# Kernel tuning notes

Measured on AMD Instinct MI355X. Metric: run time of the kernel, lower is better.

The kernel has to match this reference:

```python
import jax, jax.numpy as jnp
import numpy as np

# Rows of A/B form separable 3x3 filters via outer product:
#   f0 = identity, f1 = sobel_y, f2 = sobel_x
_A = np.array([[0, 1, 0], [1, 0, -1], [1, 2, 1]], dtype=np.float32)
_B = np.array([[0, 1, 0], [1, 2, 1], [1, 0, -1]], dtype=np.float32)
_LAP = np.array([[0, -1, 0], [-1, 4, -1], [0, -1, 0]], dtype=np.float32)  # 4-connected Laplacian


def _fixed_kernels(C):
    # separable depthwise kernels, torch grouped-conv channel-major order: out idx = c*3 + f
    sep = np.einsum('fi,fj->fij', _A, _B)                       # (3, 3, 3)
    sep_k = np.tile(sep[None], (C, 1, 1, 1)).reshape(C * 3, 1, 3, 3)
    lap_k = np.tile(_LAP[None, None], (C, 1, 1, 1))             # (C, 1, 3, 3)
    return jnp.asarray(sep_k), jnp.asarray(lap_k)


def _conv(xp, k, groups=1):
    # cross-correlation, VALID on already-padded input (matches torch F.conv2d)
    return jax.lax.conv_general_dilated(
        xp, k, window_strides=(1, 1), padding='VALID',
        dimension_numbers=('NCHW', 'OIHW', 'NCHW'),
        feature_group_count=groups)


def setup_inputs() -> dict:
    key = jax.random.key(0)
    k1, k2, k3 = jax.random.split(key, 3)
    N, C, H, W, F = 8, 64, 256, 256, 128
    x = jax.random.normal(k1, (N, C, H, W), dtype=jnp.float32)
    fan_in = C * 9
    W_learned = jax.random.uniform(k2, (F, C, 3, 3), jnp.float32,
                                   -1.0 / np.sqrt(fan_in), 1.0 / np.sqrt(fan_in))
    b_learned = jax.random.uniform(k3, (F,), jnp.float32,
                                   -1.0 / np.sqrt(fan_in), 1.0 / np.sqrt(fan_in))
    return {"x": x, "W_learned": W_learned, "b_learned": b_learned}


def reference(x, W_learned, b_learned):
    C = x.shape[1]
    sep_k, lap_k = _fixed_kernels(C)
    # replicate (edge) pad by 1 on H and W
    xp = jnp.pad(x, ((0, 0), (0, 0), (1, 1), (1, 1)), mode='edge')
    sep = _conv(xp, sep_k, groups=C)                 # (N, 3C, H, W)
    lap = _conv(xp, lap_k, groups=C)                 # (N, C,  H, W)
    learned = _conv(xp, W_learned) + b_learned[None, :, None, None]  # (N, F, H, W)
    return jnp.concatenate([sep, lap, learned], axis=1)
```

## Files before the change

### kernel.cpp

```cpp
#include <hip/hip_runtime.h>

#define HH 256
#define WW 256
#define CC 64
#define FF 128
#define NN 8
#define OUTC 384
#define HW (HH * WW)

typedef __attribute__((ext_vector_type(8))) short bf16x8;
typedef __attribute__((ext_vector_type(4))) float f32x4;

__device__ __forceinline__ int clampi(int v, int lo, int hi) {
    return v < lo ? lo : (v > hi ? hi : v);
}

static __device__ __forceinline__ unsigned short f2bf(float x) {
    unsigned u = __builtin_bit_cast(unsigned, x);
    u += 0x7FFFu + ((u >> 16) & 1u);
    return (unsigned short)(u >> 16);
}
static __device__ __forceinline__ unsigned packbf(float a, float b) {
    return (unsigned)f2bf(a) | ((unsigned)f2bf(b) << 16);
}
static __device__ __forceinline__ float bf2f(unsigned short s) {
    return __builtin_bit_cast(float, (unsigned)s << 16);
}
static __device__ __forceinline__ void nts(float* p, float a, float b, float c, float d) {
    f32x4 v = {a, b, c, d};
    __builtin_nontemporal_store(v, reinterpret_cast<f32x4*>(p));
}

__global__ __launch_bounds__(256) void wT_kernel(const float* __restrict__ Wl,
                                                 unsigned short* __restrict__ wsW) {
    int e = blockIdx.x * 256 + threadIdx.x;
    if (e >= 9216) return;
    int t = e >> 10;
    int rem = e & 1023;
    int kg = rem >> 7;
    int f = rem & 127;
    unsigned u[4];
#pragma unroll
    for (int j2 = 0; j2 < 4; ++j2) {
        float a = Wl[(size_t)f * 576 + (size_t)(kg * 8 + 2 * j2) * 9 + t];
        float b = Wl[(size_t)f * 576 + (size_t)(kg * 8 + 2 * j2 + 1) * 9 + t];
        u[j2] = packbf(a, b);
    }
    *reinterpret_cast<uint4*>(wsW + (size_t)e * 8) = make_uint4(u[0], u[1], u[2], u[3]);
}

__global__ __launch_bounds__(256) void pack_kernel(const float* __restrict__ x,
                                                   unsigned short* __restrict__ xt) {
    int b = blockIdx.x;
    int y = b & 255;
    int cg = (b >> 8) & 7;
    int n = b >> 11;
    int w = threadIdx.x;
    const float* xp = x + ((size_t)(n * CC + cg * 8)) * HW + (size_t)y * WW + w;
    unsigned u[4];
#pragma unroll
    for (int j2 = 0; j2 < 4; ++j2)
        u[j2] = packbf(xp[(size_t)(2 * j2) * HW], xp[(size_t)(2 * j2 + 1) * HW]);
    *reinterpret_cast<uint4*>(xt + ((size_t)((n * 8 + cg) * HH + y) * WW + w) * 8) =
        make_uint4(u[0], u[1], u[2], u[3]);
}

__global__ __launch_bounds__(256, 4) void learned_kernel(const unsigned short* __restrict__ wsW,
                                                         const unsigned short* __restrict__ xt,
                                                         const float* __restrict__ bl,
                                                         float* __restrict__ out) {
    __shared__ float lds_e[4][16][68];

    int q = blockIdx.x;
    int xs = q & 1;
    int y = (q >> 1) & 255;
    int n = q >> 9;

    int tid = threadIdx.x;
    int lane = tid & 63;
    int w = tid >> 6;
    int wf = w >> 1;
    int ws = w & 1;
    int x0 = xs * 128 + ws * 64;
    int lr = lane & 15;
    int lk = lane >> 4;

    const char* xb = reinterpret_cast<const char*>(xt) + (size_t)n * (8 * HH * WW * 16);

    int colb[4][3];
#pragma unroll
    for (int j = 0; j < 4; ++j)
#pragma unroll
        for (int dx = 0; dx < 3; ++dx)
            colb[j][dx] = clampi(x0 + j * 16 + lr + dx - 1, 0, WW - 1) * 16;

    f32x4 acc[4][4] = {};

#pragma unroll
    for (int t = 0; t < 9; ++t) {
        int dy = t / 3, dx = t - 3 * (t / 3);
        int yc = clampi(y + dy - 1, 0, HH - 1);
#pragma unroll
        for (int kk = 0; kk < 2; ++kk) {
            int kg = kk * 4 + lk;
            size_t rowoff = ((size_t)kg * HH + yc) * (WW * 16);
            bf16x8 a4[4], b4[4];
#pragma unroll
            for (int mt = 0; mt < 4; ++mt)
                a4[mt] = *reinterpret_cast<const bf16x8*>(
                    wsW + ((size_t)(t * 8 + kg) * 128 + wf * 64 + mt * 16 + lr) * 8);
#pragma unroll
            for (int j = 0; j < 4; ++j)
                b4[j] = *reinterpret_cast<const bf16x8*>(xb + rowoff + colb[j][dx]);
#pragma unroll
            for (int mt = 0; mt < 4; ++mt)
#pragma unroll
                for (int j = 0; j < 4; ++j)
                    acc[mt][j] = __builtin_amdgcn_mfma_f32_16x16x32_bf16(
                        a4[mt], b4[j], acc[mt][j], 0, 0, 0);
        }
    }

    float* le = &lds_e[w][0][0];
#pragma unroll
    for (int mt = 0; mt < 4; ++mt) {
#pragma unroll
        for (int i = 0; i < 4; ++i) {
            int f16 = lk * 4 + i;
            float bv = bl[wf * 64 + mt * 16 + f16];
#pragma unroll
            for (int j = 0; j < 4; ++j)
                le[f16 * 68 + j * 16 + lr] = acc[mt][j][i] + bv;
        }
#pragma unroll
        for (int p = 0; p < 4; ++p) {
            int f16 = p * 4 + lk;
            const float* s = &le[f16 * 68 + lr * 4];
            int f = wf * 64 + mt * 16 + f16;
            nts(out + (size_t)(n * OUTC + 256 + f) * HW + (size_t)y * WW + x0 + lr * 4,
                s[0], s[1], s[2], s[3]);
        }
    }
}

__global__ __launch_bounds__(256) void dw_kernel(const unsigned short* __restrict__ xt,
                                                 float* __restrict__ out) {
    int b = blockIdx.x;
    int y = b & 255;
    int cg = (b >> 8) & 7;
    int n = b >> 11;
    int w = threadIdx.x;

    const unsigned short* xg = xt + (size_t)(n * 8 + cg) * HH * WW * 8;
    int yr[3], wc[3];
#pragma unroll
    for (int d = 0; d < 3; ++d) {
        yr[d] = clampi(y + d - 1, 0, HH - 1);
        wc[d] = clampi(w + d - 1, 0, WW - 1);
    }
    uint4 chunk[3][3];
#pragma unroll
    for (int r = 0; r < 3; ++r)
#pragma unroll
        for (int c = 0; c < 3; ++c)
            chunk[r][c] = *reinterpret_cast<const uint4*>(
                xg + ((size_t)yr[r] * WW + wc[c]) * 8);

    size_t ob = (size_t)n * OUTC * HW + (size_t)y * WW + w;
#pragma unroll
    for (int j = 0; j < 8; ++j) {
        float v[3][3];
#pragma unroll
        for (int r = 0; r < 3; ++r)
#pragma unroll
            for (int c = 0; c < 3; ++c) {
                unsigned word = (&chunk[r][c].x)[j >> 1];
                v[r][c] = bf2f((unsigned short)(j & 1 ? word >> 16 : word & 0xffff));
            }
        int ch = cg * 8 + j;
        float tL = v[0][0], tC = v[0][1], tR = v[0][2];
        float mL = v[1][0], mC = v[1][1], mR = v[1][2];
        float bL = v[2][0], bC = v[2][1], bR = v[2][2];
        float o0 = mC;
        float o1 = (tL + 2.f * tC + tR) - (bL + 2.f * bC + bR);
        float o2 = (tL - tR) + 2.f * (mL - mR) + (bL - bR);
        float o3 = 4.f * mC - tC - bC - mL - mR;
        __builtin_nontemporal_store(o0, out + ob + (size_t)(ch * 3 + 0) * HW);
        __builtin_nontemporal_store(o1, out + ob + (size_t)(ch * 3 + 1) * HW);
        __builtin_nontemporal_store(o2, out + ob + (size_t)(ch * 3 + 2) * HW);
        __builtin_nontemporal_store(o3, out + ob + (size_t)(192 + ch) * HW);
    }
}

extern "C" void kernel_launch(void* const* d_in, const int* in_sizes, int n_in,
                              void* d_out, int out_size, void* d_ws, size_t ws_size,
                              hipStream_t stream) {
    const float* x  = (const float*)d_in[0];
    const float* Wl = (const float*)d_in[1];
    const float* bl = (const float*)d_in[2];
    float* out = (float*)d_out;

    unsigned short* wsW = (unsigned short*)d_ws;
    unsigned short* xt  = (unsigned short*)((char*)d_ws + 262144);

    wT_kernel<<<36, 256, 0, stream>>>(Wl, wsW);
    pack_kernel<<<16384, 256, 0, stream>>>(x, xt);
    learned_kernel<<<NN * 512, 256, 0, stream>>>(wsW, xt, bl, out);
    dw_kernel<<<16384, 256, 0, stream>>>(xt, out);
}
```

Measured before the change: 289.5 us.

## Merge learned conv and depthwise kernels into one interleaved XCD-aware launch

Combines the MFMA-based learned convolution and the memory-bound depthwise/Laplacian kernel into a single launch. Blocks are interleaved one learned block per four depthwise blocks, so compute-heavy and store-heavy work run together on the same CUs. Each batch image is mapped to one XCD via blockIdx&7 so that XCD's L2 holds that image's packed input. The cost is a larger kernel whose register and LDS footprint, set by the learned path, also limits occupancy for the depthwise blocks.

```diff
diff --git a/kernel.cpp b/kernel.cpp
--- a/kernel.cpp
+++ b/kernel.cpp
@@ -26,7 +26,7 @@
 static __device__ __forceinline__ float bf2f(unsigned short s) {
     return __builtin_bit_cast(float, (unsigned)s << 16);
 }
-static __device__ __forceinline__ void nts(float* p, float a, float b, float c, float d) {
+static __device__ __forceinline__ void nts4(float* p, float a, float b, float c, float d) {
     f32x4 v = {a, b, c, d};
     __builtin_nontemporal_store(v, reinterpret_cast<f32x4*>(p));
 }
@@ -65,130 +65,137 @@
         make_uint4(u[0], u[1], u[2], u[3]);
 }
 
-__global__ __launch_bounds__(256, 4) void learned_kernel(const unsigned short* __restrict__ wsW,
-                                                         const unsigned short* __restrict__ xt,
-                                                         const float* __restrict__ bl,
-                                                         float* __restrict__ out) {
+__global__ __launch_bounds__(256, 4) void mixed_kernel(const unsigned short* __restrict__ wsW,
+                                                       const unsigned short* __restrict__ xt,
+                                                       const float* __restrict__ bl,
+                                                       float* __restrict__ out) {
     __shared__ float lds_e[4][16][68];
 
-    int q = blockIdx.x;
-    int xs = q & 1;
-    int y = (q >> 1) & 255;
-    int n = q >> 9;
-
-    int tid = threadIdx.x;
-    int lane = tid & 63;
-    int w = tid >> 6;
-    int wf = w >> 1;
-    int ws = w & 1;
-    int x0 = xs * 128 + ws * 64;
-    int lr = lane & 15;
-    int lk = lane >> 4;
-
-    const char* xb = reinterpret_cast<const char*>(xt) + (size_t)n * (8 * HH * WW * 16);
-
-    int colb[4][3];
-#pragma unroll
-    for (int j = 0; j < 4; ++j)
-#pragma unroll
-        for (int dx = 0; dx < 3; ++dx)
-            colb[j][dx] = clampi(x0 + j * 16 + lr + dx - 1, 0, WW - 1) * 16;
-
-    f32x4 acc[4][4] = {};
-
-#pragma unroll
-    for (int t = 0; t < 9; ++t) {
-        int dy = t / 3, dx = t - 3 * (t / 3);
-        int yc = clampi(y + dy - 1, 0, HH - 1);
-#pragma unroll
-        for (int kk = 0; kk < 2; ++kk) {
-            int kg = kk * 4 + lk;
-            size_t rowoff = ((size_t)kg * HH + yc) * (WW * 16);
-            bf16x8 a4[4], b4[4];
-#pragma unroll
-            for (int mt = 0; mt < 4; ++mt)
-                a4[mt] = *reinterpret_cast<const bf16x8*>(
-                    wsW + ((size_t)(t * 8 + kg) * 128 + wf * 64 + mt * 16 + lr) * 8);
-#pragma unroll
-            for (int j = 0; j < 4; ++j)
-                b4[j] = *reinterpret_cast<const bf16x8*>(xb + rowoff + colb[j][dx]);
-#pragma unroll
-            for (int mt = 0; mt < 4; ++mt)
+    int b = blockIdx.x;
+    int g = b / 5;
+    int r = b - g * 5;
+    int xcd = b & 7;
+    int cnt = g >> 3;
+
+    if (r == 0) {
+        int n = xcd;
+        int y = cnt >> 1;
+        int xs = cnt & 1;
+
+        int tid = threadIdx.x;
+        int lane = tid & 63;
+        int w = tid >> 6;
+        int wf = w >> 1;
+        int ws = w & 1;
+        int x0 = xs * 128 + ws * 64;
+        int lr = lane & 15;
+        int lk = lane >> 4;
+
+        const char* xb = reinterpret_cast<const char*>(xt) + (size_t)n * (8 * HH * WW * 16);
+
+        int colb[4][3];
+#pragma unroll
+        for (int j = 0; j < 4; ++j)
+#pragma unroll
+            for (int dx = 0; dx < 3; ++dx)
+                colb[j][dx] = clampi(x0 + j * 16 + lr + dx - 1, 0, WW - 1) * 16;
+
+        f32x4 acc[4][4] = {};
+
+#pragma unroll
+        for (int t = 0; t < 9; ++t) {
+            int dy = t / 3, dx = t - 3 * (t / 3);
+            int yc = clampi(y + dy - 1, 0, HH - 1);
+#pragma unroll
+            for (int kk = 0; kk < 2; ++kk) {
+                int kg = kk * 4 + lk;
+                size_t rowoff = ((size_t)kg * HH + yc) * (WW * 16);
+                bf16x8 a4[4], b4[4];
+#pragma unroll
+                for (int mt = 0; mt < 4; ++mt)
+                    a4[mt] = *reinterpret_cast<const bf16x8*>(
+                        wsW + ((size_t)(t * 8 + kg) * 128 + wf * 64 + mt * 16 + lr) * 8);
 #pragma unroll
                 for (int j = 0; j < 4; ++j)
-                    acc[mt][j] = __builtin_amdgcn_mfma_f32_16x16x32_bf16(
-                        a4[mt], b4[j], acc[mt][j], 0, 0, 0);
-        }
+                    b4[j] = *reinterpret_cast<const bf16x8*>(xb + rowoff + colb[j][dx]);
+#pragma unroll
+                for (int mt = 0; mt < 4; ++mt)
+#pragma unroll
+                    for (int j = 0; j < 4; ++j)
+                        acc[mt][j] = __builtin_amdgcn_mfma_f32_16x16x32_bf16(
+                            a4[mt], b4[j], acc[mt][j], 0, 0, 0);
+            }
+        }
+
+        float* le = &lds_e[w][0][0];
+#pragma unroll
+        for (int mt = 0; mt < 4; ++mt) {
+#pragma unroll
+            for (int i = 0; i < 4; ++i) {
+                int f16 = lk * 4 + i;
+                float bv = bl[wf * 64 + mt * 16 + f16];
+#pragma unroll
+                for (int j = 0; j < 4; ++j)
+                    le[f16 * 68 + j * 16 + lr] = acc[mt][j][i] + bv;
+            }
+#pragma unroll
+            for (int p = 0; p < 4; ++p) {
+                int f16 = p * 4 + lk;
+                const float* s = &le[f16 * 68 + lr * 4];
+                int f = wf * 64 + mt * 16 + f16;
+                nts4(out + (size_t)(n * OUTC + 256 + f) * HW + (size_t)y * WW + x0 + lr * 4,
+                     s[0], s[1], s[2], s[3]);
+            }
+        }
+        return;
     }
 
-    float* le = &lds_e[w][0][0];
-#pragma unroll
-    for (int mt = 0; mt < 4; ++mt) {
-#pragma unroll
-        for (int i = 0; i < 4; ++i) {
-            int f16 = lk * 4 + i;
-            float bv = bl[wf * 64 + mt * 16 + f16];
-#pragma unroll
-            for (int j = 0; j < 4; ++j)
-                le[f16 * 68 + j * 16 + lr] = acc[mt][j][i] + bv;
-        }
-#pragma unroll
-        for (int p = 0; p < 4; ++p) {
-            int f16 = p * 4 + lk;
-            const float* s = &le[f16 * 68 + lr * 4];
-            int f = wf * 64 + mt * 16 + f16;
-            nts(out + (size_t)(n * OUTC + 256 + f) * HW + (size_t)y * WW + x0 + lr * 4,
-                s[0], s[1], s[2], s[3]);
-        }
-    }
-}
-
-__global__ __launch_bounds__(256) void dw_kernel(const unsigned short* __restrict__ xt,
-                                                 float* __restrict__ out) {
-    int b = blockIdx.x;
-    int y = b & 255;
-    int cg = (b >> 8) & 7;
-    int n = b >> 11;
-    int w = threadIdx.x;
-
-    const unsigned short* xg = xt + (size_t)(n * 8 + cg) * HH * WW * 8;
-    int yr[3], wc[3];
-#pragma unroll
-    for (int d = 0; d < 3; ++d) {
-        yr[d] = clampi(y + d - 1, 0, HH - 1);
-        wc[d] = clampi(w + d - 1, 0, WW - 1);
-    }
-    uint4 chunk[3][3];
-#pragma unroll
-    for (int r = 0; r < 3; ++r)
-#pragma unroll
-        for (int c = 0; c < 3; ++c)
-            chunk[r][c] = *reinterpret_cast<const uint4*>(
-                xg + ((size_t)yr[r] * WW + wc[c]) * 8);
-
-    size_t ob = (size_t)n * OUTC * HW + (size_t)y * WW + w;
-#pragma unroll
-    for (int j = 0; j < 8; ++j) {
-        float v[3][3];
-#pragma unroll
-        for (int r = 0; r < 3; ++r)
-#pragma unroll
-            for (int c = 0; c < 3; ++c) {
-                unsigned word = (&chunk[r][c].x)[j >> 1];
-                v[r][c] = bf2f((unsigned short)(j & 1 ? word >> 16 : word & 0xffff));
-            }
-        int ch = cg * 8 + j;
-        float tL = v[0][0], tC = v[0][1], tR = v[0][2];
-        float mL = v[1][0], mC = v[1][1], mR = v[1][2];
-        float bL = v[2][0], bC = v[2][1], bR = v[2][2];
-        float o0 = mC;
-        float o1 = (tL + 2.f * tC + tR) - (bL + 2.f * bC + bR);
-        float o2 = (tL - tR) + 2.f * (mL - mR) + (bL - bR);
-        float o3 = 4.f * mC - tC - bC - mL - mR;
-        __builtin_nontemporal_store(o0, out + ob + (size_t)(ch * 3 + 0) * HW);
-        __builtin_nontemporal_store(o1, out + ob + (size_t)(ch * 3 + 1) * HW);
-        __builtin_nontemporal_store(o2, out + ob + (size_t)(ch * 3 + 2) * HW);
-        __builtin_nontemporal_store(o3, out + ob + (size_t)(192 + ch) * HW);
+    {
+        int m = (r - 1) * 512 + cnt;
+        int n = xcd;
+        int cg = m >> 8;
+        int y = m & 255;
+        int w = threadIdx.x;
+
+        const unsigned short* xg = xt + (size_t)(n * 8 + cg) * HH * WW * 8;
+        int yr[3], wc[3];
+#pragma unroll
+        for (int d = 0; d < 3; ++d) {
+            yr[d] = clampi(y + d - 1, 0, HH - 1);
+            wc[d] = clampi(w + d - 1, 0, WW - 1);
+        }
+        uint4 chunk[3][3];
+#pragma unroll
+        for (int rr = 0; rr < 3; ++rr)
+#pragma unroll
+            for (int c = 0; c < 3; ++c)
+                chunk[rr][c] = *reinterpret_cast<const uint4*>(
+                    xg + ((size_t)yr[rr] * WW + wc[c]) * 8);
+
+        size_t ob = (size_t)n * OUTC * HW + (size_t)y * WW + w;
+#pragma unroll
+        for (int j = 0; j < 8; ++j) {
+            float v[3][3];
+#pragma unroll
+            for (int rr = 0; rr < 3; ++rr)
+#pragma unroll
+                for (int c = 0; c < 3; ++c) {
+                    unsigned word = (&chunk[rr][c].x)[j >> 1];
+                    v[rr][c] = bf2f((unsigned short)(j & 1 ? word >> 16 : word & 0xffff));
+                }
+            int ch = cg * 8 + j;
+            float tL = v[0][0], tC = v[0][1], tR = v[0][2];
+            float mL = v[1][0], mC = v[1][1], mR = v[1][2];
+            float bL = v[2][0], bC = v[2][1], bR = v[2][2];
+            float o0 = mC;
+            float o1 = (tL + 2.f * tC + tR) - (bL + 2.f * bC + bR);
+            float o2 = (tL - tR) + 2.f * (mL - mR) + (bL - bR);
+            float o3 = 4.f * mC - tC - bC - mL - mR;
+            __builtin_nontemporal_store(o0, out + ob + (size_t)(ch * 3 + 0) * HW);
+            __builtin_nontemporal_store(o1, out + ob + (size_t)(ch * 3 + 1) * HW);
+            __builtin_nontemporal_store(o2, out + ob + (size_t)(ch * 3 + 2) * HW);
+            __builtin_nontemporal_store(o3, out + ob + (size_t)(192 + ch) * HW);
+        }
     }
 }
 
@@ -205,6 +212,5 @@
 
     wT_kernel<<<36, 256, 0, stream>>>(Wl, wsW);
     pack_kernel<<<16384, 256, 0, stream>>>(x, xt);
-    learned_kernel<<<NN * 512, 256, 0, stream>>>(wsW, xt, bl, out);
-    dw_kernel<<<16384, 256, 0, stream>>>(xt, out);
-}
+    mixed_kernel<<<20480, 256, 0, stream>>>(wsW, xt, bl, out);
+}
```

Result: faster. 234.2 us (-19.1%).
